# Performance work log

Measured on AMD Instinct MI355X. Metric: run time of the kernel, lower is better.

## Reference

```python
import math
import jax, jax.numpy as jnp
import numpy as np

EPS_LN = 1e-5
EPS_NORM = 1e-12


def conv2d(x, w, b=None, groups=1):
    # x: (B,C,H,W), w: (O, I//groups, kh, kw)
    out = jax.lax.conv_general_dilated(
        x, w, window_strides=(1, 1), padding='SAME',
        dimension_numbers=('NCHW', 'OIHW', 'NCHW'),
        feature_group_count=groups)
    if b is not None:
        out = out + b[None, :, None, None]
    return out


def layernorm2d(x, w, b):
    # LayerNorm over channel dim of (B,C,H,W)
    mu = x.mean(axis=1, keepdims=True)
    var = ((x - mu) ** 2).mean(axis=1, keepdims=True)
    xn = (x - mu) / jnp.sqrt(var + EPS_LN)
    return xn * w[None, :, None, None] + b[None, :, None, None]


def l2norm(x):
    n = jnp.sqrt((x * x).sum(axis=-1, keepdims=True))
    return x / jnp.maximum(n, EPS_NORM)


def mha(s, Wi, bi, Wo, bo, num_heads):
    # torch nn.MultiheadAttention (batch_first) self-attention
    B, S, C = s.shape
    Dh = C // num_heads
    qkv = s @ Wi.T + bi                      # (B,S,3C)
    q, k, v = jnp.split(qkv, 3, axis=-1)
    hd = lambda t: t.reshape(B, S, num_heads, Dh).transpose(0, 2, 1, 3)
    q, k, v = hd(q), hd(k), hd(v)            # (B,H,S,Dh)
    attn = jax.nn.softmax(jnp.einsum('bhqd,bhkd->bhqk', q, k) / math.sqrt(Dh), axis=-1)
    o = jnp.einsum('bhqk,bhkd->bhqd', attn, v).transpose(0, 2, 1, 3).reshape(B, S, C)
    return o @ Wo.T + bo


def frfn(x, pconv_w, lin1_w, lin1_b, dw_w, dw_b, lin2_w, lin2_b):
    b, c, h, w = x.shape
    dc = c // 4
    x1 = conv2d(x[:, :dc], pconv_w)                       # partial conv, no bias
    x = jnp.concatenate([x1, x[:, dc:]], axis=1)
    xt = x.transpose(0, 2, 3, 1).reshape(b, h * w, c)
    y = jax.nn.gelu(xt @ lin1_w.T + lin1_b, approximate=False)  # (b,hw,2*hid)
    y1, y2 = jnp.split(y, 2, axis=-1)
    hid = lin1_w.shape[0] // 2
    y1 = y1.reshape(b, h, w, hid).transpose(0, 3, 1, 2)
    y1 = jax.nn.gelu(conv2d(y1, dw_w, dw_b, groups=hid), approximate=False)
    y1 = y1.transpose(0, 2, 3, 1).reshape(b, h * w, hid)
    out = (y1 * y2) @ lin2_w.T + lin2_b
    return out.reshape(b, h, w, c).transpose(0, 3, 1, 2)


def setup_inputs() -> dict:
    key = jax.random.key(0)
    ks = jax.random.split(key, 10)
    B, C, H, W = 16, 256, 64, 64
    HID = 2 * C  # FRFN hidden = embed_dim*2
    DC = C // 4
    w = lambda k, shape: (jax.random.normal(k, shape, dtype=jnp.float32) * 0.02)
    return {
        'x': jax.random.normal(ks[0], (B, C, H, W), dtype=jnp.float32),
        'slot_scale': jnp.asarray(C ** -0.5, dtype=jnp.float32),
        'norm1_w': jnp.ones((C,), jnp.float32), 'norm1_b': jnp.zeros((C,), jnp.float32),
        'in_proj_w': w(ks[1], (3 * C, C)), 'in_proj_b': jnp.zeros((3 * C,), jnp.float32),
        'out_proj_w': w(ks[2], (C, C)), 'out_proj_b': jnp.zeros((C,), jnp.float32),
        'norm2_w': jnp.ones((C,), jnp.float32), 'norm2_b': jnp.zeros((C,), jnp.float32),
        'pconv_w': w(ks[3], (DC, DC, 3, 3)),
        'lin1_w': w(ks[4], (2 * HID, C)), 'lin1_b': jnp.zeros((2 * HID,), jnp.float32),
        'dw_w': w(ks[5], (HID, 1, 3, 3)), 'dw_b': jnp.zeros((HID,), jnp.float32),
        'lin2_w': w(ks[6], (C, HID)), 'lin2_b': jnp.zeros((C,), jnp.float32),
    }


def reference(x, slot_scale, norm1_w, norm1_b, in_proj_w, in_proj_b,
              out_proj_w, out_proj_b, norm2_w, norm2_b,
              pconv_w, lin1_w, lin1_b, dw_w, dw_b, lin2_w, lin2_b):
    NUM_HEADS, POOL = 8, 8
    b, c, h, w = x.shape
    copy = x
    # ada_avgpool slot init: 8x8 exact block means (h,w divisible by pool)
    pooled = x.reshape(b, c, POOL, h // POOL, POOL, w // POOL).mean(axis=(3, 5))  # (b,c,8,8)
    init_slots = pooled.transpose(0, 2, 3, 1).reshape(b, POOL * POOL, c)          # (b,S,c)

    shortcut = x
    xn = layernorm2d(x, norm1_w, norm1_b)
    xf = xn.transpose(0, 2, 3, 1).reshape(b, h * w, c)                            # (b,N,c)
    logits = slot_scale * jnp.einsum('bsc,bnc->bsn', l2norm(init_slots), l2norm(xf))
    slots = jnp.einsum('bsn,bnc->bsc', jax.nn.softmax(logits, axis=-1), xf)
    slots = mha(slots, in_proj_w, in_proj_b, out_proj_w, out_proj_b, NUM_HEADS)
    out = jnp.einsum('bns,bsc->bnc', jax.nn.softmax(logits.transpose(0, 2, 1), axis=-1), slots)
    out = out.transpose(0, 2, 1).reshape(b, c, h, w)

    x = shortcut + out
    x = x + frfn(layernorm2d(x, norm2_w, norm2_b),
                 pconv_w, lin1_w, lin1_b, dw_w, dw_b, lin2_w, lin2_b)
    return (x, copy - x)
```

## Files before the change

kernel.cpp:

```cpp
#include <hip/hip_runtime.h>
#include <hip/hip_bf16.h>
#include <stdint.h>
#include <math.h>

#define BB 16
#define CC 256
#define HH 64
#define WW 64
#define NN 4096
#define SS 64
#define NHEAD 8
#define DH 32
#define HID 512
#define DC 64

typedef float    f32x4  __attribute__((ext_vector_type(4)));
typedef uint16_t u16x8  __attribute__((ext_vector_type(8)));
typedef uint16_t u16x4  __attribute__((ext_vector_type(4)));
typedef uint16_t u16x2  __attribute__((ext_vector_type(2)));

__device__ __forceinline__ float geluf(float x){
  return 0.5f * x * (1.0f + erff(x * 0.70710678118654752f));
}
__device__ __forceinline__ uint16_t f2b(float f){
  union { float f; uint32_t u; } v; v.f = f;
  uint32_t r = v.u + 0x7fffu + ((v.u >> 16) & 1u);
  return (uint16_t)(r >> 16);
}
__device__ __forceinline__ float b2f(uint16_t h){
  union { uint32_t u; float f; } v; v.u = ((uint32_t)h) << 16;
  return v.f;
}

__device__ __forceinline__ float waveSum(float v){
#pragma unroll
  for (int m = 32; m >= 1; m >>= 1) v += __shfl_xor(v, m, 64);
  return v;
}
__device__ __forceinline__ float blockSum256(float v, float* s4){
  v = waveSum(v);
  __syncthreads();
  if ((threadIdx.x & 63) == 0) s4[threadIdx.x >> 6] = v;
  __syncthreads();
  return s4[0] + s4[1] + s4[2] + s4[3];
}

__device__ __forceinline__ void g2l16(const void* g, void* l){
  __builtin_amdgcn_global_load_lds((const __attribute__((address_space(1))) uint32_t*)g,
                                   (__attribute__((address_space(3))) uint32_t*)l, 16, 0, 0);
}

__device__ __forceinline__ void mfma_bf16(f32x4& d, u16x8 a, u16x8 b){
  asm volatile("v_mfma_f32_16x16x32_bf16 %0, %1, %2, %0" : "+v"(d) : "v"(a), "v"(b));
}

__device__ __forceinline__ void mma_core(const uint16_t* lA, int lda, const uint16_t* lB, int ldb,
                                         f32x4 (&acc)[4][4], int wrow, int wcol, int lane){
  const int rb = lane & 15, kb = (lane >> 4) * 8;
#pragma unroll
  for (int ks = 0; ks < 2; ks++){
    u16x8 af[4], bf[4];
#pragma unroll
    for (int m = 0; m < 4; m++)
      af[m] = *(const u16x8*)&lA[(wrow + m * 16 + rb) * lda + ks * 32 + kb];
#pragma unroll
    for (int n = 0; n < 4; n++)
      bf[n] = *(const u16x8*)&lB[(wcol + n * 16 + rb) * ldb + ks * 32 + kb];
#pragma unroll
    for (int m = 0; m < 4; m++)
#pragma unroll
      for (int n = 0; n < 4; n++)
        mfma_bf16(acc[m][n], af[m], bf[n]);
  }
}

__global__ __launch_bounds__(256) void k_t2b(const float* __restrict__ in, uint16_t* __restrict__ out){
  __shared__ float tile[64][33];
  int b = blockIdx.z;
  int n0 = blockIdx.x * 32;
  int c0 = blockIdx.y * 64;
  int tx = threadIdx.x, ty = threadIdx.y;
  const float* src = in + (size_t)b * CC * NN;
#pragma unroll
  for (int i = 0; i < 64; i += 8)
    tile[ty + i][tx] = src[(size_t)(c0 + ty + i) * NN + n0 + tx];
  __syncthreads();
  uint16_t* dst = out + (size_t)b * NN * CC;
#pragma unroll
  for (int i = 0; i < 32; i += 8){
    int r = ty + i;
    u16x2 o; o[0] = f2b(tile[tx * 2][r]); o[1] = f2b(tile[tx * 2 + 1][r]);
    *(u16x2*)&dst[(size_t)(n0 + r) * CC + c0 + tx * 2] = o;
  }
}

__global__ __launch_bounds__(256) void k_pool(const uint16_t* __restrict__ xhwcb, uint16_t* __restrict__ slotsNb){
  int bs = blockIdx.x; int b = bs >> 6, s = bs & 63;
  int sy = (s >> 3) * 8, sx = (s & 7) * 8;
  int t = threadIdx.x;
  int c4 = t & 63, pg = t >> 6;
  const uint16_t* base = xhwcb + (size_t)b * NN * CC;
  float a0 = 0.f, a1 = 0.f, a2 = 0.f, a3 = 0.f;
#pragma unroll
  for (int i = 0; i < 16; i++){
    int p = pg * 16 + i; int py = p >> 3, px = p & 7;
    u16x4 v = *(const u16x4*)&base[(size_t)((sy + py) * WW + sx + px) * CC + c4 * 4];
    a0 += b2f(v[0]); a1 += b2f(v[1]); a2 += b2f(v[2]); a3 += b2f(v[3]);
  }
  __shared__ float sm[4][64][4];
  sm[pg][c4][0] = a0; sm[pg][c4][1] = a1; sm[pg][c4][2] = a2; sm[pg][c4][3] = a3;
  __syncthreads();
  if (t < 64){
    float v0 = (sm[0][t][0] + sm[1][t][0] + sm[2][t][0] + sm[3][t][0]) * (1.0f / 64.0f);
    float v1 = (sm[0][t][1] + sm[1][t][1] + sm[2][t][1] + sm[3][t][1]) * (1.0f / 64.0f);
    float v2 = (sm[0][t][2] + sm[1][t][2] + sm[2][t][2] + sm[3][t][2]) * (1.0f / 64.0f);
    float v3 = (sm[0][t][3] + sm[1][t][3] + sm[2][t][3] + sm[3][t][3]) * (1.0f / 64.0f);
    float ss = waveSum(v0 * v0 + v1 * v1 + v2 * v2 + v3 * v3);
    float inv = 1.0f / fmaxf(sqrtf(ss), 1e-12f);
    u16x4 o; o[0] = f2b(v0 * inv); o[1] = f2b(v1 * inv); o[2] = f2b(v2 * inv); o[3] = f2b(v3 * inv);
    *(u16x4*)&slotsNb[(size_t)bs * CC + t * 4] = o;
  }
}

__global__ __launch_bounds__(256) void k_ln_w(const uint16_t* __restrict__ xa, const uint16_t* __restrict__ xb,
                                              const float* __restrict__ w, const float* __restrict__ b,
                                              uint16_t* __restrict__ xoutb, float* __restrict__ rn,
                                              uint16_t* __restrict__ xn2p){
  int row = blockIdx.x * 4 + (threadIdx.x >> 6);
  int lane = threadIdx.x & 63;
  u16x4 va = *(const u16x4*)&xa[(size_t)row * CC + lane * 4];
  float v0 = b2f(va[0]), v1 = b2f(va[1]), v2 = b2f(va[2]), v3 = b2f(va[3]);
  if (xb){
    u16x4 vb = *(const u16x4*)&xb[(size_t)row * CC + lane * 4];
    v0 += b2f(vb[0]); v1 += b2f(vb[1]); v2 += b2f(vb[2]); v3 += b2f(vb[3]);
  }
  float mu = waveSum(v0 + v1 + v2 + v3) * (1.0f / CC);
  float d0 = v0 - mu, d1 = v1 - mu, d2 = v2 - mu, d3 = v3 - mu;
  float var = waveSum(d0 * d0 + d1 * d1 + d2 * d2 + d3 * d3) * (1.0f / CC);
  float inv = rsqrtf(var + 1e-5f);
  float4 wv = *(const float4*)&w[lane * 4];
  float4 bv = *(const float4*)&b[lane * 4];
  float x0 = d0 * inv * wv.x + bv.x;
  float x1 = d1 * inv * wv.y + bv.y;
  float x2 = d2 * inv * wv.z + bv.z;
  float x3 = d3 * inv * wv.w + bv.w;
  u16x4 o; o[0] = f2b(x0); o[1] = f2b(x1); o[2] = f2b(x2); o[3] = f2b(x3);
  *(u16x4*)&xoutb[(size_t)row * CC + lane * 4] = o;
  if (xn2p && lane < 16){
    int bb = row >> 12, n = row & 4095, y = n >> 6, x = n & 63;
    *(u16x4*)&xn2p[(((size_t)(bb * 66 + y + 1)) * 66 + x + 1) * 64 + lane * 4] = o;
  }
  if (rn){
    float ss = waveSum(x0 * x0 + x1 * x1 + x2 * x2 + x3 * x3);
    if (lane == 0) rn[row] = 1.0f / fmaxf(sqrtf(ss), 1e-12f);
  }
}

__global__ __launch_bounds__(256) void k_zb(uint16_t* __restrict__ xn2p){
  int i = blockIdx.x * 256 + threadIdx.x;
  if (i >= 16 * 260 * 16) return;
  int c4 = i & 15; int rest = i >> 4;
  int j = rest % 260; int b = rest / 260;
  int py, px;
  if (j < 66){ py = 0; px = j; }
  else if (j < 132){ py = 65; px = j - 66; }
  else if (j < 196){ py = j - 132 + 1; px = 0; }
  else { py = j - 196 + 1; px = 65; }
  u16x4 z; z[0] = 0; z[1] = 0; z[2] = 0; z[3] = 0;
  *(u16x4*)&xn2p[(((size_t)(b * 66 + py)) * 66 + px) * 64 + c4 * 4] = z;
}

__global__ __launch_bounds__(256) void k_cvtw(const float* __restrict__ wi, const float* __restrict__ wo,
                                              const float* __restrict__ w1, const float* __restrict__ w2,
                                              const float* __restrict__ pw, const float* __restrict__ dww,
                                              uint16_t* __restrict__ wib, uint16_t* __restrict__ wob,
                                              uint16_t* __restrict__ w1b, uint16_t* __restrict__ w2b,
                                              uint16_t* __restrict__ wp2, float* __restrict__ dwwT){
  int i = blockIdx.x * 256 + threadIdx.x;
  if (i < 163840){
    const float* src; uint16_t* dst; int off;
    if (i < 49152){ src = wi; dst = wib; off = i; }
    else if (i < 65536){ src = wo; dst = wob; off = i - 49152; }
    else if (i < 131072){ src = w1; dst = w1b; off = i - 65536; }
    else { src = w2; dst = w2b; off = i - 131072; }
    float4 v = ((const float4*)src)[off];
    u16x4 o;
    o[0] = f2b(v.x); o[1] = f2b(v.y); o[2] = f2b(v.z); o[3] = f2b(v.w);
    *(u16x4*)&dst[(size_t)off * 4] = o;
  } else if (i < 200704){
    int j = i - 163840;
    if (j < 64 * 576){
      int co = j / 576, r = j % 576, tap = r >> 6, ci = r & 63;
      wp2[j] = f2b(pw[(size_t)co * 576 + ci * 9 + tap]);
    }
  } else {
    int j = i - 200704;
    if (j < 9 * HID){
      int tap = j / HID, ch = j % HID;
      dwwT[j] = dww[(size_t)ch * 9 + tap];
    }
  }
}

__global__ __launch_bounds__(256) void k_logits_mfma(const uint16_t* __restrict__ slotsNb,
                                                     const uint16_t* __restrict__ xnb,
                                                     const float* __restrict__ rn,
                                                     const float* __restrict__ scale_p,
                                                     uint16_t* __restrict__ E){
  __shared__ uint16_t smem[20480];
  __shared__ float rnS[256];
  uint16_t* lA = smem;
  uint16_t* lB = smem + 64 * 64;
  int t = threadIdx.x, lane = t & 63, w = t >> 6;
  int b = blockIdx.y, n0 = blockIdx.x * 256;
  rnS[t] = rn[b * NN + n0 + t];
  f32x4 acc[4][4];
#pragma unroll
  for (int m = 0; m < 4; m++)
#pragma unroll
    for (int n = 0; n < 4; n++) acc[m][n] = (f32x4){0.f, 0.f, 0.f, 0.f};
  for (int kc = 0; kc < 4; kc++){
#pragma unroll
    for (int i = 0; i < 2; i++){
      int idx = i * 256 + t, row = idx >> 3, kp = idx & 7;
      *(u16x8*)&lA[row * 64 + kp * 8] = *(const u16x8*)&slotsNb[(size_t)(b * 64 + row) * 256 + kc * 64 + kp * 8];
    }
#pragma unroll
    for (int i = 0; i < 8; i++){
      int idx = i * 256 + t, row = idx >> 3, kp = idx & 7;
      *(u16x8*)&lB[row * 64 + kp * 8] = *(const u16x8*)&xnb[((size_t)b * NN + n0 + row) * 256 + kc * 64 + kp * 8];
    }
    __syncthreads();
    mma_core(lA, 64, lB, 64, acc, 0, w * 64, lane);
    __syncthreads();
  }
  float scale = scale_p[0];
  int rb4 = (lane >> 4) * 4, cb = lane & 15;
#pragma unroll
  for (int m = 0; m < 4; m++)
#pragma unroll
    for (int n = 0; n < 4; n++)
#pragma unroll
      for (int j = 0; j < 4; j++){
        int s = m * 16 + rb4 + j, nl = w * 64 + n * 16 + cb;
        smem[s * 264 + nl] = f2b(expf(acc[m][n][j] * scale * rnS[nl]));
      }
  __syncthreads();
#pragma unroll
  for (int i = 0; i < 8; i++){
    int idx = i * 256 + t, row = idx >> 5, cseg = idx & 31;
    *(u16x8*)&E[((size_t)b * 64 + row) * NN + n0 + cseg * 8] = *(const u16x8*)&smem[row * 264 + cseg * 8];
  }
}

__global__ __launch_bounds__(256) void k_z1(const uint16_t* __restrict__ E, float* __restrict__ invz1){
  int bs = blockIdx.x, t = threadIdx.x;
  const uint16_t* row = E + (size_t)bs * NN + t * 16;
  float s = 0.f;
#pragma unroll
  for (int i = 0; i < 16; i++) s += b2f(row[i]);
  __shared__ float s4[4];
  float z = blockSum256(s, s4);
  if (t == 0) invz1[bs] = 1.0f / z;
}

__global__ __launch_bounds__(256) void k_slots_mfma(const uint16_t* __restrict__ E,
                                                    const uint16_t* __restrict__ xnb,
                                                    float* __restrict__ part){
  __shared__ uint16_t lA[64 * 64];
  __shared__ uint16_t lB[256 * 72];
  int t = threadIdx.x, lane = t & 63, w = t >> 6;
  int ks = blockIdx.x, b = blockIdx.y;
  f32x4 acc[4][4];
#pragma unroll
  for (int m = 0; m < 4; m++)
#pragma unroll
    for (int n = 0; n < 4; n++) acc[m][n] = (f32x4){0.f, 0.f, 0.f, 0.f};
  for (int kc = 0; kc < 8; kc++){
    int n0 = ks * 512 + kc * 64;
#pragma unroll
    for (int i = 0; i < 2; i++){
      int idx = i * 256 + t, row = idx >> 3, kp = idx & 7;
      *(u16x8*)&lA[row * 64 + kp * 8] = *(const u16x8*)&E[((size_t)b * 64 + row) * NN + n0 + kp * 8];
    }
#pragma unroll
    for (int i = 0; i < 8; i++){
      int idx = i * 256 + t, nrow = idx >> 5, cseg = idx & 31;
      u16x8 v = *(const u16x8*)&xnb[((size_t)b * NN + n0 + nrow) * 256 + cseg * 8];
#pragma unroll
      for (int j = 0; j < 8; j++) lB[(cseg * 8 + j) * 72 + nrow] = v[j];
    }
    __syncthreads();
    mma_core(lA, 64, lB, 72, acc, 0, w * 64, lane);
    __syncthreads();
  }
  int rb4 = (lane >> 4) * 4, cb = lane & 15;
#pragma unroll
  for (int m = 0; m < 4; m++)
#pragma unroll
    for (int n = 0; n < 4; n++)
#pragma unroll
      for (int j = 0; j < 4; j++){
        int s = m * 16 + rb4 + j, c = w * 64 + n * 16 + cb;
        part[(((size_t)b * 8 + ks) * 64 + s) * 256 + c] = acc[m][n][j];
      }
}

__global__ __launch_bounds__(256) void k_fold(const float* __restrict__ part, const float* __restrict__ invz1,
                                              uint16_t* __restrict__ slotsb){
  int i = blockIdx.x * 256 + threadIdx.x;
  int row = i >> 6, c4 = i & 63;
  int b = row >> 6, s = row & 63;
  float4 a = {0.f, 0.f, 0.f, 0.f};
#pragma unroll
  for (int p = 0; p < 8; p++){
    float4 v = *(const float4*)&part[(((size_t)b * 8 + p) * 64 + s) * 256 + c4 * 4];
    a.x += v.x; a.y += v.y; a.z += v.z; a.w += v.w;
  }
  float iz = invz1[row];
  u16x4 o; o[0] = f2b(a.x * iz); o[1] = f2b(a.y * iz); o[2] = f2b(a.z * iz); o[3] = f2b(a.w * iz);
  *(u16x4*)&slotsb[(size_t)row * 256 + c4 * 4] = o;
}

__global__ __launch_bounds__(256) void k_gemm_qkv(const uint16_t* __restrict__ slotsb,
                                                  const uint16_t* __restrict__ wib,
                                                  const float* __restrict__ bi,
                                                  float* __restrict__ qkv){
  __shared__ uint16_t lA[128 * 64];
  __shared__ uint16_t lB[128 * 64];
  int t = threadIdx.x, lane = t & 63, w = t >> 6;
  int wrow = (w >> 1) * 64, wcol = (w & 1) * 64;
  int BR = blockIdx.x * 128, BC = blockIdx.y * 128;
  f32x4 acc[4][4];
#pragma unroll
  for (int m = 0; m < 4; m++)
#pragma unroll
    for (int n = 0; n < 4; n++) acc[m][n] = (f32x4){0.f, 0.f, 0.f, 0.f};
  for (int kc = 0; kc < 4; kc++){
#pragma unroll
    for (int i = 0; i < 4; i++){
      int idx = i * 256 + t, row = idx >> 3, kp = idx & 7;
      *(u16x8*)&lA[row * 64 + kp * 8] = *(const u16x8*)&slotsb[(size_t)(BR + row) * 256 + kc * 64 + kp * 8];
      *(u16x8*)&lB[row * 64 + kp * 8] = *(const u16x8*)&wib[(size_t)(BC + row) * 256 + kc * 64 + kp * 8];
    }
    __syncthreads();
    mma_core(lA, 64, lB, 64, acc, wrow, wcol, lane);
    __syncthreads();
  }
  int rb4 = (lane >> 4) * 4, cb = lane & 15;
#pragma unroll
  for (int m = 0; m < 4; m++)
#pragma unroll
    for (int n = 0; n < 4; n++){
      int c = BC + wcol + n * 16 + cb;
      float bias = bi[c];
#pragma unroll
      for (int j = 0; j < 4; j++)
        qkv[(size_t)(BR + wrow + m * 16 + rb4 + j) * 768 + c] = acc[m][n][j] + bias;
    }
}

__global__ __launch_bounds__(256) void k_attn(const float* __restrict__ qkv, uint16_t* __restrict__ aob){
  int b = blockIdx.x >> 3, h = blockIdx.x & 7;
  __shared__ float lq[64][33], lk[64][33], lv[64][33];
  __shared__ float sc[64][65];
  int t = threadIdx.x;
  for (int idx = t; idx < 64 * 32; idx += 256){
    int s = idx >> 5, d = idx & 31;
    const float* base = qkv + ((size_t)b * SS + s) * 768 + h * DH + d;
    lq[s][d] = base[0];
    lk[s][d] = base[256];
    lv[s][d] = base[512];
  }
  __syncthreads();
  const float rs = 0.17677669529663687f;
  for (int idx = t; idx < 64 * 64; idx += 256){
    int qq = idx >> 6, kk = idx & 63;
    float a = 0.f;
#pragma unroll
    for (int d = 0; d < 32; d++) a += lq[qq][d] * lk[kk][d];
    sc[qq][kk] = a * rs;
  }
  __syncthreads();
  {
    int r = t >> 2, sub = t & 3;
    float m = -1e30f;
#pragma unroll
    for (int k = sub * 16; k < sub * 16 + 16; k++) m = fmaxf(m, sc[r][k]);
    m = fmaxf(m, __shfl_xor(m, 1, 64));
    m = fmaxf(m, __shfl_xor(m, 2, 64));
    float z = 0.f;
#pragma unroll
    for (int k = sub * 16; k < sub * 16 + 16; k++){
      float e = expf(sc[r][k] - m); sc[r][k] = e; z += e;
    }
    z += __shfl_xor(z, 1, 64);
    z += __shfl_xor(z, 2, 64);
    float iv = 1.0f / z;
#pragma unroll
    for (int k = sub * 16; k < sub * 16 + 16; k++) sc[r][k] *= iv;
  }
  __syncthreads();
  for (int idx = t; idx < 64 * 32; idx += 256){
    int qq = idx >> 5, d = idx & 31;
    float a = 0.f;
#pragma unroll
    for (int k = 0; k < 64; k++) a += sc[qq][k] * lv[k][d];
    aob[((size_t)b * SS + qq) * CC + h * DH + d] = f2b(a);
  }
}

__global__ __launch_bounds__(256) void k_gemm_oproj(const uint16_t* __restrict__ aob,
                                                    const uint16_t* __restrict__ wob,
                                                    const float* __restrict__ bo,
                                                    uint16_t* __restrict__ sl2Tb){
  __shared__ uint16_t lA[128 * 64];
  __shared__ uint16_t lB[128 * 64];
  int t = threadIdx.x, lane = t & 63, w = t >> 6;
  int wrow = (w >> 1) * 64, wcol = (w & 1) * 64;
  int BR = blockIdx.x * 128, BC = blockIdx.y * 128;
  f32x4 acc[4][4];
#pragma unroll
  for (int m = 0; m < 4; m++)
#pragma unroll
    for (int n = 0; n < 4; n++) acc[m][n] = (f32x4){0.f, 0.f, 0.f, 0.f};
  for (int kc = 0; kc < 4; kc++){
#pragma unroll
    for (int i = 0; i < 4; i++){
      int idx = i * 256 + t, row = idx >> 3, kp = idx & 7;
      *(u16x8*)&lA[row * 64 + kp * 8] = *(const u16x8*)&aob[(size_t)(BR + row) * 256 + kc * 64 + kp * 8];
      *(u16x8*)&lB[row * 64 + kp * 8] = *(const u16x8*)&wob[(size_t)(BC + row) * 256 + kc * 64 + kp * 8];
    }
    __syncthreads();
    mma_core(lA, 64, lB, 64, acc, wrow, wcol, lane);
    __syncthreads();
  }
  int rb4 = (lane >> 4) * 4, cb = lane & 15;
#pragma unroll
  for (int m = 0; m < 4; m++)
#pragma unroll
    for (int n = 0; n < 4; n++){
      int c = BC + wcol + n * 16 + cb;
      float bias = bo[c];
#pragma unroll
      for (int j = 0; j < 4; j++){
        int r = BR + wrow + m * 16 + rb4 + j;
        int b = r >> 6, s = r & 63;
        sl2Tb[((size_t)b * 256 + c) * 64 + s] = f2b(acc[m][n][j] + bias);
      }
    }
}

__global__ __launch_bounds__(256) void k_mix(const uint16_t* __restrict__ E, const uint16_t* __restrict__ sl2Tb,
                                             uint16_t* __restrict__ mixb){
  __shared__ uint16_t lA[128 * 72];
  __shared__ uint16_t lB[128 * 64];
  __shared__ float z2S[128];
  int t = threadIdx.x, lane = t & 63, w = t >> 6;
  int wrow = (w >> 1) * 64, wcol = (w & 1) * 64;
  int BR = blockIdx.x * 128, BC = blockIdx.y * 128, b = blockIdx.z;
#pragma unroll
  for (int i = 0; i < 4; i++){
    int idx = i * 256 + t; int s = idx >> 4, n8 = (idx & 15) * 8;
    u16x8 v = *(const u16x8*)&E[((size_t)b * 64 + s) * NN + BR + n8];
#pragma unroll
    for (int j = 0; j < 8; j++) lA[(n8 + j) * 72 + s] = v[j];
  }
#pragma unroll
  for (int i = 0; i < 4; i++){
    int idx = i * 256 + t, row = idx >> 3, kp = idx & 7;
    *(u16x8*)&lB[row * 64 + kp * 8] = *(const u16x8*)&sl2Tb[((size_t)b * 256 + BC + row) * 64 + kp * 8];
  }
  __syncthreads();
  if (t < 128){
    float s = 0.f;
#pragma unroll
    for (int k2 = 0; k2 < 64; k2++) s += b2f(lA[t * 72 + k2]);
    z2S[t] = 1.0f / s;
  }
  __syncthreads();
  f32x4 acc[4][4];
#pragma unroll
  for (int m = 0; m < 4; m++)
#pragma unroll
    for (int n = 0; n < 4; n++) acc[m][n] = (f32x4){0.f, 0.f, 0.f, 0.f};
  mma_core(lA, 72, lB, 64, acc, wrow, wcol, lane);
  int rb4 = (lane >> 4) * 4, cb = lane & 15;
#pragma unroll
  for (int m = 0; m < 4; m++)
#pragma unroll
    for (int n = 0; n < 4; n++)
#pragma unroll
      for (int j = 0; j < 4; j++){
        int lrow = wrow + m * 16 + rb4 + j;
        size_t gi = ((size_t)b * NN + BR + lrow) * 256 + BC + wcol + n * 16 + cb;
        mixb[gi] = f2b(acc[m][n][j] * z2S[lrow]);
      }
}

__global__ __launch_bounds__(256) void k_pconv_mfma(const uint16_t* __restrict__ xn2p,
                                                    const uint16_t* __restrict__ wp2,
                                                    uint16_t* __restrict__ pcb){
  __shared__ uint16_t lA[256 * 64];
  __shared__ uint16_t lB[64 * 64];
  int t = threadIdx.x, lane = t & 63, w = t >> 6;
  int wrow = w * 64;
  int BR = blockIdx.x * 256;
  f32x4 acc[4][4];
#pragma unroll
  for (int m = 0; m < 4; m++)
#pragma unroll
    for (int n = 0; n < 4; n++) acc[m][n] = (f32x4){0.f, 0.f, 0.f, 0.f};
  for (int tap = 0; tap < 9; tap++){
    int dy = tap / 3 - 1, dx = tap % 3 - 1;
#pragma unroll
    for (int i = 0; i < 8; i++){
      int q = (w * 8 + i) * 64 + lane;
      int row = q >> 3, kpe = (q & 7) * 8;
      int r = BR + row;
      int b = r >> 12, n = r & 4095, y = n >> 6, x = n & 63;
      size_t p = ((size_t)(b * 66 + (y + 1 + dy)) * 66 + (x + 1 + dx)) * 64 + kpe;
      g2l16(&xn2p[p], &lA[(w * 8 + i) * 512]);
    }
#pragma unroll
    for (int i = 0; i < 2; i++){
      int q = (w * 2 + i) * 64 + lane;
      int row = q >> 3, kpe = (q & 7) * 8;
      g2l16(&wp2[(size_t)row * 576 + tap * 64 + kpe], &lB[(w * 2 + i) * 512]);
    }
    __syncthreads();
    mma_core(lA, 64, lB, 64, acc, wrow, 0, lane);
    __syncthreads();
  }
  int rb4 = (lane >> 4) * 4, cb = lane & 15;
#pragma unroll
  for (int m = 0; m < 4; m++)
#pragma unroll
    for (int n = 0; n < 4; n++)
#pragma unroll
      for (int j = 0; j < 4; j++)
        pcb[(size_t)(BR + wrow + m * 16 + rb4 + j) * 64 + (n * 16 + cb)] = f2b(acc[m][n][j]);
}

__global__ __launch_bounds__(256) void k_lin1_mfma(const uint16_t* __restrict__ pcb,
                                                   const uint16_t* __restrict__ xn2b,
                                                   const uint16_t* __restrict__ w1b,
                                                   const float* __restrict__ b1,
                                                   uint16_t* __restrict__ Y1b, uint16_t* __restrict__ Y2b){
  __shared__ uint16_t lA[128 * 64];
  __shared__ uint16_t lB[128 * 64];
  int t = threadIdx.x, lane = t & 63, w = t >> 6;
  int wrow = (w >> 1) * 64, wcol = (w & 1) * 64;
  int BC = blockIdx.x * 128, BR = blockIdx.y * 128;
  f32x4 acc[4][4];
#pragma unroll
  for (int m = 0; m < 4; m++)
#pragma unroll
    for (int n = 0; n < 4; n++) acc[m][n] = (f32x4){0.f, 0.f, 0.f, 0.f};
  for (int kc = 0; kc < 4; kc++){
#pragma unroll
    for (int i = 0; i < 4; i++){
      int q = (w * 4 + i) * 64 + lane;
      int row = q >> 3, kpe = (q & 7) * 8;
      size_t gr = (size_t)(BR + row);
      const uint16_t* src = (kc == 0) ? &pcb[gr * 64 + kpe] : &xn2b[gr * 256 + kc * 64 + kpe];
      g2l16(src, &lA[(w * 4 + i) * 512]);
      g2l16(&w1b[(size_t)(BC + row) * 256 + kc * 64 + kpe], &lB[(w * 4 + i) * 512]);
    }
    __syncthreads();
    mma_core(lA, 64, lB, 64, acc, wrow, wcol, lane);
    __syncthreads();
  }
  int rb4 = (lane >> 4) * 4, cb = lane & 15;
#pragma unroll
  for (int m = 0; m < 4; m++){
#pragma unroll
    for (int n = 0; n < 4; n++){
      int c = BC + wcol + n * 16 + cb;
      float bias = b1[c];
#pragma unroll
      for (int j = 0; j < 4; j++){
        size_t r = (size_t)(BR + wrow + m * 16 + rb4 + j);
        uint16_t h = f2b(geluf(acc[m][n][j] + bias));
        if (c < HID) Y1b[r * HID + c] = h;
        else         Y2b[r * HID + (c - HID)] = h;
      }
    }
  }
}

__global__ __launch_bounds__(256) void k_dwconv(const uint16_t* __restrict__ Y1b,
                                                const float* __restrict__ dwwT,
                                                const float* __restrict__ dwb,
                                                const uint16_t* __restrict__ Y2b,
                                                uint16_t* __restrict__ YPb){
  int b = blockIdx.y;
  int t = threadIdx.x;
  int n = blockIdx.x * 4 + (t >> 6);
  int cg = (t & 63) * 8;
  int y = n >> 6, x = n & 63;
  const uint16_t* base = Y1b + (size_t)b * NN * HID;
  float acc[8];
  {
    float4 b0 = *(const float4*)&dwb[cg];
    float4 b1 = *(const float4*)&dwb[cg + 4];
    acc[0] = b0.x; acc[1] = b0.y; acc[2] = b0.z; acc[3] = b0.w;
    acc[4] = b1.x; acc[5] = b1.y; acc[6] = b1.z; acc[7] = b1.w;
  }
#pragma unroll
  for (int ky = 0; ky < 3; ky++){
    int iy = y + ky - 1; if (iy < 0 || iy >= HH) continue;
#pragma unroll
    for (int kx = 0; kx < 3; kx++){
      int ix = x + kx - 1; if (ix < 0 || ix >= WW) continue;
      u16x8 v = *(const u16x8*)&base[(size_t)(iy * WW + ix) * HID + cg];
      const float* wt = &dwwT[(ky * 3 + kx) * HID + cg];
      float4 w0 = *(const float4*)wt;
      float4 w1 = *(const float4*)(wt + 4);
      acc[0] += b2f(v[0]) * w0.x; acc[1] += b2f(v[1]) * w0.y;
      acc[2] += b2f(v[2]) * w0.z; acc[3] += b2f(v[3]) * w0.w;
      acc[4] += b2f(v[4]) * w1.x; acc[5] += b2f(v[5]) * w1.y;
      acc[6] += b2f(v[6]) * w1.z; acc[7] += b2f(v[7]) * w1.w;
    }
  }
  u16x8 y2 = *(const u16x8*)&Y2b[((size_t)b * NN + n) * HID + cg];
  u16x8 o;
#pragma unroll
  for (int j = 0; j < 8; j++) o[j] = f2b(geluf(acc[j]) * b2f(y2[j]));
  *(u16x8*)&YPb[((size_t)b * NN + n) * HID + cg] = o;
}

__global__ __launch_bounds__(256) void k_lin2_mfma(const uint16_t* __restrict__ YPb,
                                                   const uint16_t* __restrict__ w2b,
                                                   const float* __restrict__ b2,
                                                   uint16_t* __restrict__ deltab){
  __shared__ uint16_t lA[128 * 64];
  __shared__ uint16_t lB[128 * 64];
  int t = threadIdx.x, lane = t & 63, w = t >> 6;
  int wrow = (w >> 1) * 64, wcol = (w & 1) * 64;
  int BC = blockIdx.x * 128, BR = blockIdx.y * 128;
  f32x4 acc[4][4];
#pragma unroll
  for (int m = 0; m < 4; m++)
#pragma unroll
    for (int n = 0; n < 4; n++) acc[m][n] = (f32x4){0.f, 0.f, 0.f, 0.f};
  for (int kc = 0; kc < 8; kc++){
#pragma unroll
    for (int i = 0; i < 4; i++){
      int q = (w * 4 + i) * 64 + lane;
      int row = q >> 3, kpe = (q & 7) * 8;
      g2l16(&YPb[(size_t)(BR + row) * HID + kc * 64 + kpe], &lA[(w * 4 + i) * 512]);
      g2l16(&w2b[(size_t)(BC + row) * HID + kc * 64 + kpe], &lB[(w * 4 + i) * 512]);
    }
    __syncthreads();
    mma_core(lA, 64, lB, 64, acc, wrow, wcol, lane);
    __syncthreads();
  }
  int rb4 = (lane >> 4) * 4, cb = lane & 15;
#pragma unroll
  for (int m = 0; m < 4; m++){
#pragma unroll
    for (int n = 0; n < 4; n++){
      int c = BC + wcol + n * 16 + cb;
      float bias = b2[c];
#pragma unroll
      for (int j = 0; j < 4; j++){
        size_t gr = (size_t)(BR + wrow + m * 16 + rb4 + j);
        deltab[gr * CC + c] = f2b(acc[m][n][j] + bias);
      }
    }
  }
}

__global__ __launch_bounds__(256) void k_final2(const uint16_t* __restrict__ mixb,
                                                const uint16_t* __restrict__ deltab,
                                                const uint16_t* __restrict__ xhwcb,
                                                float* __restrict__ out){
  __shared__ float t0[64 * 68];
  __shared__ float t1[64 * 68];
  int b = blockIdx.z;
  int n0 = blockIdx.x * 64, c0 = blockIdx.y * 64;
  int t = threadIdx.x;
#pragma unroll
  for (int i = 0; i < 4; i++){
    int idx = i * 256 + t, row = idx >> 4, c4 = idx & 15;
    size_t gp = ((size_t)b * NN + n0 + row) * CC + c0 + c4 * 4;
    u16x4 m = *(const u16x4*)&mixb[gp];
    u16x4 d = *(const u16x4*)&deltab[gp];
    u16x4 xh = *(const u16x4*)&xhwcb[gp];
    f32x4 v0, v1;
#pragma unroll
    for (int j = 0; j < 4; j++){
      float v = b2f(m[j]) + b2f(d[j]);
      v0[j] = b2f(xh[j]) + v;
      v1[j] = -v;
    }
    *(f32x4*)&t0[row * 68 + c4 * 4] = v0;
    *(f32x4*)&t1[row * 68 + c4 * 4] = v1;
  }
  __syncthreads();
  int cl = t >> 2, seg = t & 3;
  float* o1 = out + (size_t)BB * CC * NN;
  size_t gbase = ((size_t)(b * CC + c0 + cl)) * NN + n0 + seg * 16;
#pragma unroll
  for (int k = 0; k < 4; k++){
    float4 a, c;
    a.x = t0[(seg * 16 + k * 4 + 0) * 68 + cl];
    a.y = t0[(seg * 16 + k * 4 + 1) * 68 + cl];
    a.z = t0[(seg * 16 + k * 4 + 2) * 68 + cl];
    a.w = t0[(seg * 16 + k * 4 + 3) * 68 + cl];
    c.x = t1[(seg * 16 + k * 4 + 0) * 68 + cl];
    c.y = t1[(seg * 16 + k * 4 + 1) * 68 + cl];
    c.z = t1[(seg * 16 + k * 4 + 2) * 68 + cl];
    c.w = t1[(seg * 16 + k * 4 + 3) * 68 + cl];
    *(float4*)&out[gbase + k * 4] = a;
    *(float4*)&o1[gbase + k * 4] = c;
  }
}

extern "C" void kernel_launch(void* const* d_in, const int* in_sizes, int n_in,
                              void* d_out, int out_size, void* d_ws, size_t ws_size,
                              hipStream_t stream){
  const float* x       = (const float*)d_in[0];
  const float* scale_p = (const float*)d_in[1];
  const float* n1w     = (const float*)d_in[2];
  const float* n1b     = (const float*)d_in[3];
  const float* wi      = (const float*)d_in[4];
  const float* bi      = (const float*)d_in[5];
  const float* wo      = (const float*)d_in[6];
  const float* bo      = (const float*)d_in[7];
  const float* n2w     = (const float*)d_in[8];
  const float* n2b     = (const float*)d_in[9];
  const float* pw      = (const float*)d_in[10];
  const float* w1      = (const float*)d_in[11];
  const float* b1      = (const float*)d_in[12];
  const float* dww     = (const float*)d_in[13];
  const float* dwb     = (const float*)d_in[14];
  const float* w2      = (const float*)d_in[15];
  const float* b2      = (const float*)d_in[16];

  float* base = (float*)d_ws;
  size_t off = 0;
  float* part = base + off; off += (size_t)BB * 8 * SS * CC;
  float* QKV  = base + off; off += (size_t)BB * SS * 3 * CC;
  float* RN   = base + off; off += (size_t)BB * NN;
  float* IZ1  = base + off; off += (size_t)BB * SS;
  float* dwwT = base + off; off += (size_t)9 * HID;
  uint16_t* slotsNb = (uint16_t*)(base + off); off += (size_t)BB * SS * CC / 2;
  uint16_t* slotsb  = (uint16_t*)(base + off); off += (size_t)BB * SS * CC / 2;
  uint16_t* aob     = (uint16_t*)(base + off); off += (size_t)BB * SS * CC / 2;
  uint16_t* sl2Tb   = (uint16_t*)(base + off); off += (size_t)BB * CC * SS / 2;
  uint16_t* xhwcb   = (uint16_t*)(base + off); off += (size_t)BB * NN * CC / 2;
  uint16_t* xnb     = (uint16_t*)(base + off); off += (size_t)BB * NN * CC / 2;
  uint16_t* mixb    = (uint16_t*)(base + off); off += (size_t)BB * NN * CC / 2;
  uint16_t* deltab  = (uint16_t*)(base + off); off += (size_t)BB * NN * CC / 2;
  uint16_t* E       = (uint16_t*)(base + off); off += (size_t)BB * SS * NN / 2;
  uint16_t* w1b     = (uint16_t*)(base + off); off += (size_t)(2 * HID) * CC / 2;
  uint16_t* w2b     = (uint16_t*)(base + off); off += (size_t)CC * HID / 2;
  uint16_t* wib     = (uint16_t*)(base + off); off += (size_t)(3 * CC) * CC / 2;
  uint16_t* wob     = (uint16_t*)(base + off); off += (size_t)CC * CC / 2;
  uint16_t* wp2     = (uint16_t*)(base + off); off += (size_t)64 * 576 / 2 + 16;
  uint16_t* Y1b     = (uint16_t*)(base + off); off += (size_t)BB * NN * HID / 2;
  uint16_t* Y2b     = (uint16_t*)(base + off); off += (size_t)BB * NN * HID / 2;
  uint16_t* YPb     = (uint16_t*)(base + off); off += (size_t)BB * NN * HID / 2;
  uint16_t* xn2b    = (uint16_t*)(base + off); off += (size_t)BB * NN * CC / 2;
  uint16_t* xn2p    = (uint16_t*)(base + off); off += (size_t)BB * 66 * 66 * 64 / 2;
  uint16_t* pcb     = (uint16_t*)(base + off); off += (size_t)BB * NN * 64 / 2;
  if (ws_size < off * sizeof(float)) return;
  float* OUT = (float*)d_out;

  dim3 tb2(32, 8);
  k_t2b<<<dim3(NN / 32, CC / 64, BB), tb2, 0, stream>>>(x, xhwcb);
  k_pool<<<BB * SS, 256, 0, stream>>>(xhwcb, slotsNb);
  k_ln_w<<<BB * NN / 4, 256, 0, stream>>>(xhwcb, (const uint16_t*)nullptr, n1w, n1b, xnb, RN,
                                          (uint16_t*)nullptr);
  k_cvtw<<<803, 256, 0, stream>>>(wi, wo, w1, w2, pw, dww, wib, wob, w1b, w2b, wp2, dwwT);
  k_zb<<<(16 * 260 * 16 + 255) / 256, 256, 0, stream>>>(xn2p);
  k_logits_mfma<<<dim3(NN / 256, BB), 256, 0, stream>>>(slotsNb, xnb, RN, scale_p, E);
  k_z1<<<BB * SS, 256, 0, stream>>>(E, IZ1);
  k_slots_mfma<<<dim3(8, BB), 256, 0, stream>>>(E, xnb, part);
  k_fold<<<(BB * SS * CC / 4) / 256, 256, 0, stream>>>(part, IZ1, slotsb);
  k_gemm_qkv<<<dim3(8, 6), 256, 0, stream>>>(slotsb, wib, bi, QKV);
  k_attn<<<BB * NHEAD, 256, 0, stream>>>(QKV, aob);
  k_gemm_oproj<<<dim3(8, 2), 256, 0, stream>>>(aob, wob, bo, sl2Tb);
  k_mix<<<dim3(NN / 128, CC / 128, BB), 256, 0, stream>>>(E, sl2Tb, mixb);
  k_ln_w<<<BB * NN / 4, 256, 0, stream>>>(xhwcb, mixb, n2w, n2b, xn2b, (float*)nullptr, xn2p);
  k_pconv_mfma<<<BB * NN / 256, 256, 0, stream>>>(xn2p, wp2, pcb);
  k_lin1_mfma<<<dim3(8, BB * NN / 128), 256, 0, stream>>>(pcb, xn2b, w1b, b1, Y1b, Y2b);
  k_dwconv<<<dim3(NN / 4, BB), 256, 0, stream>>>(Y1b, dwwT, dwb, Y2b, YPb);
  k_lin2_mfma<<<dim3(2, BB * NN / 128), 256, 0, stream>>>(YPb, w2b, b2, deltab);
  k_final2<<<dim3(NN / 64, CC / 64, BB), 256, 0, stream>>>(mixb, deltab, xhwcb, OUT);
}
```

Measured before the change: 502.1 us.

## Swizzle LDS tiles for MFMA GEMMs and remap lin1/lin2 blocks per XCD

Applies an XOR swizzle of the 16-byte k-chunk index by the low three row bits to the LDS tiles of all MFMA GEMM kernels. The fragment reads in mma_core use the matching swizzle through template flags, which is meant to remove LDS bank conflicts. The lin1 and lin2 launches become 1D grids that map each XCD to a contiguous range of row tiles, so the A-panel reuse stays within one L2. k_z1 also switches to vectorized 16-byte loads.

```diff
diff --git a/kernel.cpp b/kernel.cpp
--- a/kernel.cpp
+++ b/kernel.cpp
@@ -50,22 +50,32 @@
                                    (__attribute__((address_space(3))) uint32_t*)l, 16, 0, 0);
 }
 
+__device__ __forceinline__ int swz8(int row, int kp){ return (kp ^ (row & 7)) << 3; }
+
 __device__ __forceinline__ void mfma_bf16(f32x4& d, u16x8 a, u16x8 b){
   asm volatile("v_mfma_f32_16x16x32_bf16 %0, %1, %2, %0" : "+v"(d) : "v"(a), "v"(b));
 }
 
+template<int SWA, int SWB>
 __device__ __forceinline__ void mma_core(const uint16_t* lA, int lda, const uint16_t* lB, int ldb,
                                          f32x4 (&acc)[4][4], int wrow, int wcol, int lane){
-  const int rb = lane & 15, kb = (lane >> 4) * 8;
+  const int rb = lane & 15, ub = lane >> 4;
 #pragma unroll
   for (int ks = 0; ks < 2; ks++){
+    const int u = ks * 4 + ub;
     u16x8 af[4], bf[4];
 #pragma unroll
-    for (int m = 0; m < 4; m++)
-      af[m] = *(const u16x8*)&lA[(wrow + m * 16 + rb) * lda + ks * 32 + kb];
-#pragma unroll
-    for (int n = 0; n < 4; n++)
-      bf[n] = *(const u16x8*)&lB[(wcol + n * 16 + rb) * ldb + ks * 32 + kb];
+    for (int m = 0; m < 4; m++){
+      int r = wrow + m * 16 + rb;
+      int e = SWA ? ((u ^ (r & 7)) << 3) : (u << 3);
+      af[m] = *(const u16x8*)&lA[r * lda + e];
+    }
+#pragma unroll
+    for (int n = 0; n < 4; n++){
+      int r = wcol + n * 16 + rb;
+      int e = SWB ? ((u ^ (r & 7)) << 3) : (u << 3);
+      bf[n] = *(const u16x8*)&lB[r * ldb + e];
+    }
 #pragma unroll
     for (int m = 0; m < 4; m++)
 #pragma unroll
@@ -223,15 +233,15 @@
 #pragma unroll
     for (int i = 0; i < 2; i++){
       int idx = i * 256 + t, row = idx >> 3, kp = idx & 7;
-      *(u16x8*)&lA[row * 64 + kp * 8] = *(const u16x8*)&slotsNb[(size_t)(b * 64 + row) * 256 + kc * 64 + kp * 8];
+      *(u16x8*)&lA[row * 64 + swz8(row, kp)] = *(const u16x8*)&slotsNb[(size_t)(b * 64 + row) * 256 + kc * 64 + kp * 8];
     }
 #pragma unroll
     for (int i = 0; i < 8; i++){
       int idx = i * 256 + t, row = idx >> 3, kp = idx & 7;
-      *(u16x8*)&lB[row * 64 + kp * 8] = *(const u16x8*)&xnb[((size_t)b * NN + n0 + row) * 256 + kc * 64 + kp * 8];
-    }
-    __syncthreads();
-    mma_core(lA, 64, lB, 64, acc, 0, w * 64, lane);
+      *(u16x8*)&lB[row * 64 + swz8(row, kp)] = *(const u16x8*)&xnb[((size_t)b * NN + n0 + row) * 256 + kc * 64 + kp * 8];
+    }
+    __syncthreads();
+    mma_core<1, 1>(lA, 64, lB, 64, acc, 0, w * 64, lane);
     __syncthreads();
   }
   float scale = scale_p[0];
@@ -255,10 +265,11 @@
 
 __global__ __launch_bounds__(256) void k_z1(const uint16_t* __restrict__ E, float* __restrict__ invz1){
   int bs = blockIdx.x, t = threadIdx.x;
-  const uint16_t* row = E + (size_t)bs * NN + t * 16;
+  u16x8 v0 = *(const u16x8*)&E[(size_t)bs * NN + t * 16];
+  u16x8 v1 = *(const u16x8*)&E[(size_t)bs * NN + t * 16 + 8];
   float s = 0.f;
 #pragma unroll
-  for (int i = 0; i < 16; i++) s += b2f(row[i]);
+  for (int i = 0; i < 8; i++) s += b2f(v0[i]) + b2f(v1[i]);
   __shared__ float s4[4];
   float z = blockSum256(s, s4);
   if (t == 0) invz1[bs] = 1.0f / z;
@@ -281,7 +292,7 @@
 #pragma unroll
     for (int i = 0; i < 2; i++){
       int idx = i * 256 + t, row = idx >> 3, kp = idx & 7;
-      *(u16x8*)&lA[row * 64 + kp * 8] = *(const u16x8*)&E[((size_t)b * 64 + row) * NN + n0 + kp * 8];
+      *(u16x8*)&lA[row * 64 + swz8(row, kp)] = *(const u16x8*)&E[((size_t)b * 64 + row) * NN + n0 + kp * 8];
     }
 #pragma unroll
     for (int i = 0; i < 8; i++){
@@ -291,7 +302,7 @@
       for (int j = 0; j < 8; j++) lB[(cseg * 8 + j) * 72 + nrow] = v[j];
     }
     __syncthreads();
-    mma_core(lA, 64, lB, 72, acc, 0, w * 64, lane);
+    mma_core<1, 0>(lA, 64, lB, 72, acc, 0, w * 64, lane);
     __syncthreads();
   }
   int rb4 = (lane >> 4) * 4, cb = lane & 15;
@@ -340,11 +351,11 @@
 #pragma unroll
     for (int i = 0; i < 4; i++){
       int idx = i * 256 + t, row = idx >> 3, kp = idx & 7;
-      *(u16x8*)&lA[row * 64 + kp * 8] = *(const u16x8*)&slotsb[(size_t)(BR + row) * 256 + kc * 64 + kp * 8];
-      *(u16x8*)&lB[row * 64 + kp * 8] = *(const u16x8*)&wib[(size_t)(BC + row) * 256 + kc * 64 + kp * 8];
-    }
-    __syncthreads();
-    mma_core(lA, 64, lB, 64, acc, wrow, wcol, lane);
+      *(u16x8*)&lA[row * 64 + swz8(row, kp)] = *(const u16x8*)&slotsb[(size_t)(BR + row) * 256 + kc * 64 + kp * 8];
+      *(u16x8*)&lB[row * 64 + swz8(row, kp)] = *(const u16x8*)&wib[(size_t)(BC + row) * 256 + kc * 64 + kp * 8];
+    }
+    __syncthreads();
+    mma_core<1, 1>(lA, 64, lB, 64, acc, wrow, wcol, lane);
     __syncthreads();
   }
   int rb4 = (lane >> 4) * 4, cb = lane & 15;
@@ -428,11 +439,11 @@
 #pragma unroll
     for (int i = 0; i < 4; i++){
       int idx = i * 256 + t, row = idx >> 3, kp = idx & 7;
-      *(u16x8*)&lA[row * 64 + kp * 8] = *(const u16x8*)&aob[(size_t)(BR + row) * 256 + kc * 64 + kp * 8];
-      *(u16x8*)&lB[row * 64 + kp * 8] = *(const u16x8*)&wob[(size_t)(BC + row) * 256 + kc * 64 + kp * 8];
-    }
-    __syncthreads();
-    mma_core(lA, 64, lB, 64, acc, wrow, wcol, lane);
+      *(u16x8*)&lA[row * 64 + swz8(row, kp)] = *(const u16x8*)&aob[(size_t)(BR + row) * 256 + kc * 64 + kp * 8];
+      *(u16x8*)&lB[row * 64 + swz8(row, kp)] = *(const u16x8*)&wob[(size_t)(BC + row) * 256 + kc * 64 + kp * 8];
+    }
+    __syncthreads();
+    mma_core<1, 1>(lA, 64, lB, 64, acc, wrow, wcol, lane);
     __syncthreads();
   }
   int rb4 = (lane >> 4) * 4, cb = lane & 15;
@@ -469,7 +480,7 @@
 #pragma unroll
   for (int i = 0; i < 4; i++){
     int idx = i * 256 + t, row = idx >> 3, kp = idx & 7;
-    *(u16x8*)&lB[row * 64 + kp * 8] = *(const u16x8*)&sl2Tb[((size_t)b * 256 + BC + row) * 64 + kp * 8];
+    *(u16x8*)&lB[row * 64 + swz8(row, kp)] = *(const u16x8*)&sl2Tb[((size_t)b * 256 + BC + row) * 64 + kp * 8];
   }
   __syncthreads();
   if (t < 128){
@@ -484,7 +495,7 @@
   for (int m = 0; m < 4; m++)
 #pragma unroll
     for (int n = 0; n < 4; n++) acc[m][n] = (f32x4){0.f, 0.f, 0.f, 0.f};
-  mma_core(lA, 72, lB, 64, acc, wrow, wcol, lane);
+  mma_core<0, 1>(lA, 72, lB, 64, acc, wrow, wcol, lane);
   int rb4 = (lane >> 4) * 4, cb = lane & 15;
 #pragma unroll
   for (int m = 0; m < 4; m++)
@@ -516,7 +527,7 @@
 #pragma unroll
     for (int i = 0; i < 8; i++){
       int q = (w * 8 + i) * 64 + lane;
-      int row = q >> 3, kpe = (q & 7) * 8;
+      int row = q >> 3, kpe = swz8(row, q & 7);
       int r = BR + row;
       int b = r >> 12, n = r & 4095, y = n >> 6, x = n & 63;
       size_t p = ((size_t)(b * 66 + (y + 1 + dy)) * 66 + (x + 1 + dx)) * 64 + kpe;
@@ -525,11 +536,11 @@
 #pragma unroll
     for (int i = 0; i < 2; i++){
       int q = (w * 2 + i) * 64 + lane;
-      int row = q >> 3, kpe = (q & 7) * 8;
+      int row = q >> 3, kpe = swz8(row, q & 7);
       g2l16(&wp2[(size_t)row * 576 + tap * 64 + kpe], &lB[(w * 2 + i) * 512]);
     }
     __syncthreads();
-    mma_core(lA, 64, lB, 64, acc, wrow, 0, lane);
+    mma_core<1, 1>(lA, 64, lB, 64, acc, wrow, 0, lane);
     __syncthreads();
   }
   int rb4 = (lane >> 4) * 4, cb = lane & 15;
@@ -551,7 +562,10 @@
   __shared__ uint16_t lB[128 * 64];
   int t = threadIdx.x, lane = t & 63, w = t >> 6;
   int wrow = (w >> 1) * 64, wcol = (w & 1) * 64;
-  int BC = blockIdx.x * 128, BR = blockIdx.y * 128;
+  int bid = blockIdx.x;
+  int xcd = bid & 7, i5 = bid >> 3;
+  int BR = (xcd * 64 + (i5 >> 3)) * 128;
+  int BC = (i5 & 7) * 128;
   f32x4 acc[4][4];
 #pragma unroll
   for (int m = 0; m < 4; m++)
@@ -561,14 +575,14 @@
 #pragma unroll
     for (int i = 0; i < 4; i++){
       int q = (w * 4 + i) * 64 + lane;
-      int row = q >> 3, kpe = (q & 7) * 8;
+      int row = q >> 3, kpe = swz8(row, q & 7);
       size_t gr = (size_t)(BR + row);
       const uint16_t* src = (kc == 0) ? &pcb[gr * 64 + kpe] : &xn2b[gr * 256 + kc * 64 + kpe];
       g2l16(src, &lA[(w * 4 + i) * 512]);
       g2l16(&w1b[(size_t)(BC + row) * 256 + kc * 64 + kpe], &lB[(w * 4 + i) * 512]);
     }
     __syncthreads();
-    mma_core(lA, 64, lB, 64, acc, wrow, wcol, lane);
+    mma_core<1, 1>(lA, 64, lB, 64, acc, wrow, wcol, lane);
     __syncthreads();
   }
   int rb4 = (lane >> 4) * 4, cb = lane & 15;
@@ -638,7 +652,10 @@
   __shared__ uint16_t lB[128 * 64];
   int t = threadIdx.x, lane = t & 63, w = t >> 6;
   int wrow = (w >> 1) * 64, wcol = (w & 1) * 64;
-  int BC = blockIdx.x * 128, BR = blockIdx.y * 128;
+  int bid = blockIdx.x;
+  int xcd = bid & 7, i5 = bid >> 3;
+  int BR = (xcd * 64 + (i5 >> 1)) * 128;
+  int BC = (i5 & 1) * 128;
   f32x4 acc[4][4];
 #pragma unroll
   for (int m = 0; m < 4; m++)
@@ -648,12 +665,12 @@
 #pragma unroll
     for (int i = 0; i < 4; i++){
       int q = (w * 4 + i) * 64 + lane;
-      int row = q >> 3, kpe = (q & 7) * 8;
+      int row = q >> 3, kpe = swz8(row, q & 7);
       g2l16(&YPb[(size_t)(BR + row) * HID + kc * 64 + kpe], &lA[(w * 4 + i) * 512]);
       g2l16(&w2b[(size_t)(BC + row) * HID + kc * 64 + kpe], &lB[(w * 4 + i) * 512]);
     }
     __syncthreads();
-    mma_core(lA, 64, lB, 64, acc, wrow, wcol, lane);
+    mma_core<1, 1>(lA, 64, lB, 64, acc, wrow, wcol, lane);
     __syncthreads();
   }
   int rb4 = (lane >> 4) * 4, cb = lane & 15;
@@ -786,8 +803,8 @@
   k_mix<<<dim3(NN / 128, CC / 128, BB), 256, 0, stream>>>(E, sl2Tb, mixb);
   k_ln_w<<<BB * NN / 4, 256, 0, stream>>>(xhwcb, mixb, n2w, n2b, xn2b, (float*)nullptr, xn2p);
   k_pconv_mfma<<<BB * NN / 256, 256, 0, stream>>>(xn2p, wp2, pcb);
-  k_lin1_mfma<<<dim3(8, BB * NN / 128), 256, 0, stream>>>(pcb, xn2b, w1b, b1, Y1b, Y2b);
+  k_lin1_mfma<<<4096, 256, 0, stream>>>(pcb, xn2b, w1b, b1, Y1b, Y2b);
   k_dwconv<<<dim3(NN / 4, BB), 256, 0, stream>>>(Y1b, dwwT, dwb, Y2b, YPb);
-  k_lin2_mfma<<<dim3(2, BB * NN / 128), 256, 0, stream>>>(YPb, w2b, b2, deltab);
+  k_lin2_mfma<<<1024, 256, 0, stream>>>(YPb, w2b, b2, deltab);
   k_final2<<<dim3(NN / 64, CC / 64, BB), 256, 0, stream>>>(mixb, deltab, xhwcb, OUT);
 }
```

Result: faster. 478.6 us (-4.7%).
